# Kernel optimization log

Measured on AMD Instinct MI355X. Metric: run time of the kernel, lower is better.

Reference implementation:

```python
import jax, jax.numpy as jnp
import numpy as np

H, C = 8, 32          # heads, per-head channels (h_feats)
NEG_SLOPE = 0.2


def setup_inputs() -> dict:
    key = jax.random.key(0)
    ks = jax.random.split(key, 9)
    N, E, F_IN, F_E = 50000, 800000, 128, 16
    x = jax.random.normal(ks[0], (N, F_IN), jnp.float32)
    edge_index = jax.random.randint(ks[1], (2, E), 0, N, jnp.int64)
    edge_attr = jax.random.normal(ks[2], (E, F_E), jnp.float32)
    s = 1.0 / np.sqrt(F_IN)
    W = jax.random.normal(ks[3], (H * C, F_IN), jnp.float32) * s
    W_edge = jax.random.normal(ks[4], (H * C, F_E), jnp.float32) * (1.0 / np.sqrt(F_E))
    att_src = jax.random.normal(ks[5], (H, C), jnp.float32) * (1.0 / np.sqrt(C))
    att_dst = jax.random.normal(ks[6], (H, C), jnp.float32) * (1.0 / np.sqrt(C))
    att_edge = jax.random.normal(ks[7], (H, C), jnp.float32) * (1.0 / np.sqrt(C))
    bias = jnp.zeros((C,), jnp.float32)
    return {"x": x, "edge_index": edge_index, "edge_attr": edge_attr,
            "W": W, "W_edge": W_edge, "att_src": att_src, "att_dst": att_dst,
            "att_edge": att_edge, "bias": bias}


def reference(x, edge_index, edge_attr, W, W_edge, att_src, att_dst, att_edge, bias):
    N = x.shape[0]
    src, dst = edge_index[0], edge_index[1]

    # --- add self loops, edge_attr fill_value='mean' (per-dst mean of incoming attrs) ---
    deg = jax.ops.segment_sum(jnp.ones_like(dst, dtype=edge_attr.dtype), dst, num_segments=N)
    loop_attr = jax.ops.segment_sum(edge_attr, dst, num_segments=N) / jnp.maximum(deg, 1.0)[:, None]
    loop = jnp.arange(N, dtype=src.dtype)
    src = jnp.concatenate([src, loop])
    dst = jnp.concatenate([dst, loop])
    ea = jnp.concatenate([edge_attr, loop_attr], axis=0)  # [E+N, F_e]

    # --- node projection and per-node attention terms ---
    xh = (x @ W.T).reshape(N, H, C)                      # [N,H,C]
    a_src = jnp.einsum('nhc,hc->nh', xh, att_src)        # [N,H]
    a_dst = jnp.einsum('nhc,hc->nh', xh, att_dst)        # [N,H]

    # edge attention folded: (lin_edge(e).view(E,H,C) * att_edge).sum(-1) == e @ M
    M = jnp.einsum('hcf,hc->fh', W_edge.reshape(H, C, -1), att_edge)  # [F_e,H]
    a_edge = ea @ M                                      # [E+N,H]

    alpha = a_src[src] + a_dst[dst] + a_edge             # [E+N,H]
    alpha = jnp.where(alpha >= 0, alpha, NEG_SLOPE * alpha)

    # --- scatter-softmax over edges grouped by dst node ---
    amax = jax.ops.segment_max(alpha, dst, num_segments=N)  # every node has a self loop
    ex = jnp.exp(alpha - amax[dst])
    denom = jax.ops.segment_sum(ex, dst, num_segments=N)
    att = ex / denom[dst]                                # [E+N,H]

    # --- weighted message scatter-sum ---
    msg = xh[src] * att[..., None]                       # [E+N,H,C]
    out = jax.ops.segment_sum(msg, dst, num_segments=N)  # [N,H,C]
    return out.mean(axis=1) + bias                       # concat=False -> head mean
```

## Files before the change

### kernel.cpp

```cpp
#include <hip/hip_runtime.h>
#include <math.h>

#define H 8
#define C 32
#define HC 256
#define FE 16
#define FIN 128
#define NEG_SLOPE 0.2f

typedef __attribute__((ext_vector_type(8))) short bf16x8;
typedef __attribute__((ext_vector_type(4))) float f32x4;

__device__ __forceinline__ unsigned short f2bf(float f) {
  unsigned int u = __float_as_uint(f);
  unsigned int lsb = (u >> 16) & 1u;
  u += 0x7fffu + lsb;
  return (unsigned short)(u >> 16);
}
__device__ __forceinline__ float bf2f(unsigned short s) {
  return __uint_as_float(((unsigned int)s) << 16);
}

__device__ __forceinline__ void split8(const float* v, bf16x8& hi, bf16x8& lo) {
#pragma unroll
  for (int i = 0; i < 8; ++i) {
    unsigned int u = __float_as_uint(v[i]);
    unsigned int hu = u & 0xffff0000u;
    float r = v[i] - __uint_as_float(hu);
    hi[i] = (short)(hu >> 16);
    lo[i] = (short)f2bf(r);
  }
}

__global__ __launch_bounds__(256) void k_xh(const float* __restrict__ x,
                                            const unsigned short* __restrict__ Whi,
                                            const unsigned short* __restrict__ Wlo,
                                            const float* __restrict__ att_src,
                                            const float* __restrict__ att_dst,
                                            unsigned short* __restrict__ xhb,
                                            float* __restrict__ a_src,
                                            float* __restrict__ a_dst, int N) {
  int t = threadIdx.x;
  int w = t >> 6, lane = t & 63;
  int n15 = lane & 15, q = lane >> 4;
  int nodeBase = blockIdx.x * 128 + w * 32;
  int chBase = blockIdx.y * 128;

  f32x4 acc[8][2];
#pragma unroll
  for (int mt = 0; mt < 8; ++mt)
#pragma unroll
    for (int nt = 0; nt < 2; ++nt) acc[mt][nt] = (f32x4)(0.f);

  for (int ks = 0; ks < 4; ++ks) {
    int kOff = ks * 32 + q * 8;
    bf16x8 Bhi[2], Blo[2];
#pragma unroll
    for (int nt = 0; nt < 2; ++nt) {
      int node = nodeBase + nt * 16 + n15;
      int rn = (node < N) ? node : (N - 1);
      const float* px = &x[(size_t)rn * FIN + kOff];
      float vb[8];
      *(float4*)&vb[0] = *(const float4*)px;
      *(float4*)&vb[4] = *(const float4*)(px + 4);
      split8(vb, Bhi[nt], Blo[nt]);
    }
#pragma unroll
    for (int mt = 0; mt < 8; ++mt) {
      int widx = ((chBase + mt * 16 + n15) << 7) + kOff;
      bf16x8 Ahi = *(const bf16x8*)&Whi[widx];
      bf16x8 Alo = *(const bf16x8*)&Wlo[widx];
#pragma unroll
      for (int nt = 0; nt < 2; ++nt) {
        acc[mt][nt] = __builtin_amdgcn_mfma_f32_16x16x32_bf16(Ahi, Bhi[nt], acc[mt][nt], 0, 0, 0);
        acc[mt][nt] = __builtin_amdgcn_mfma_f32_16x16x32_bf16(Ahi, Blo[nt], acc[mt][nt], 0, 0, 0);
        acc[mt][nt] = __builtin_amdgcn_mfma_f32_16x16x32_bf16(Alo, Bhi[nt], acc[mt][nt], 0, 0, 0);
      }
    }
  }

  float ps[2][4] = {{0.f,0.f,0.f,0.f},{0.f,0.f,0.f,0.f}};
  float pd[2][4] = {{0.f,0.f,0.f,0.f},{0.f,0.f,0.f,0.f}};
#pragma unroll
  for (int mt = 0; mt < 8; ++mt) {
    int hl = mt >> 1;
#pragma unroll
    for (int r = 0; r < 4; ++r) {
      int ch = chBase + mt * 16 + q * 4 + r;
      float as_c = att_src[ch], ad_c = att_dst[ch];
#pragma unroll
      for (int nt = 0; nt < 2; ++nt) {
        float val = acc[mt][nt][r];
        ps[nt][hl] = fmaf(val, as_c, ps[nt][hl]);
        pd[nt][hl] = fmaf(val, ad_c, pd[nt][hl]);
      }
    }
#pragma unroll
    for (int nt = 0; nt < 2; ++nt) {
      int node = nodeBase + nt * 16 + n15;
      if (node < N) {
        ushort4 us;
        us.x = f2bf(acc[mt][nt][0]); us.y = f2bf(acc[mt][nt][1]);
        us.z = f2bf(acc[mt][nt][2]); us.w = f2bf(acc[mt][nt][3]);
        *(ushort4*)&xhb[(size_t)node * HC + chBase + mt * 16 + q * 4] = us;
      }
    }
  }
#pragma unroll
  for (int nt = 0; nt < 2; ++nt)
#pragma unroll
    for (int hl = 0; hl < 4; ++hl) {
      ps[nt][hl] += __shfl_xor(ps[nt][hl], 16, 64);
      ps[nt][hl] += __shfl_xor(ps[nt][hl], 32, 64);
      pd[nt][hl] += __shfl_xor(pd[nt][hl], 16, 64);
      pd[nt][hl] += __shfl_xor(pd[nt][hl], 32, 64);
    }
  if (q == 0) {
#pragma unroll
    for (int nt = 0; nt < 2; ++nt) {
      int node = nodeBase + nt * 16 + n15;
      if (node < N) {
        *(float4*)&a_src[node * H + blockIdx.y * 4] = make_float4(ps[nt][0], ps[nt][1], ps[nt][2], ps[nt][3]);
        *(float4*)&a_dst[node * H + blockIdx.y * 4] = make_float4(pd[nt][0], pd[nt][1], pd[nt][2], pd[nt][3]);
      }
    }
  }
}

__global__ __launch_bounds__(256) void k_deg(const int* __restrict__ ei,
                                             int* __restrict__ deg,
                                             int* __restrict__ rank,
                                             const float* __restrict__ W,
                                             unsigned short* __restrict__ Whi,
                                             unsigned short* __restrict__ Wlo, int E) {
  int e = blockIdx.x * 256 + threadIdx.x;
  if (e < HC * FIN) {
    float v = W[e];
    unsigned int u = __float_as_uint(v);
    unsigned int hu = u & 0xffff0000u;
    Whi[e] = (unsigned short)(hu >> 16);
    Wlo[e] = f2bf(v - __uint_as_float(hu));
  }
  if (e < E) rank[e] = atomicAdd(&deg[ei[E + e]], 1);
}

__global__ __launch_bounds__(256) void k_scan1(const int* __restrict__ deg,
                                               int* __restrict__ bsum, int N) {
  int t = threadIdx.x;
  int i = blockIdx.x * 256 + t;
  int v = (i < N) ? deg[i] : 0;
#pragma unroll
  for (int m = 1; m < 64; m <<= 1) v += __shfl_xor(v, m, 64);
  __shared__ int wsum[4];
  if ((t & 63) == 0) wsum[t >> 6] = v;
  __syncthreads();
  if (t == 0) bsum[blockIdx.x] = wsum[0] + wsum[1] + wsum[2] + wsum[3];
}

__global__ __launch_bounds__(256) void k_scan23(const int* __restrict__ deg,
                                                const int* __restrict__ bsum,
                                                int* __restrict__ rowptr, int N, int E, int nb) {
  __shared__ int sb[256];
  __shared__ int buf[256];
  int t = threadIdx.x;
  sb[t] = (t < nb) ? bsum[t] : 0;
  int i = blockIdx.x * 256 + t;
  int v = (i < N) ? deg[i] : 0;
  buf[t] = v;
  __syncthreads();
  for (int off = 1; off < 256; off <<= 1) {
    int y1 = (t >= off) ? sb[t - off] : 0;
    int y2 = (t >= off) ? buf[t - off] : 0;
    __syncthreads();
    sb[t] += y1;
    buf[t] += y2;
    __syncthreads();
  }
  int bofs = (blockIdx.x == 0) ? 0 : sb[blockIdx.x - 1];
  if (i < N) rowptr[i] = bofs + buf[t] - v;
  if (i == 0) rowptr[N] = E;
}

__global__ __launch_bounds__(256) void k_edge_scatter(const int* __restrict__ ei,
                                                      const float* __restrict__ ea,
                                                      const float* __restrict__ W_edge,
                                                      const float* __restrict__ att_edge,
                                                      const int* __restrict__ rowptr,
                                                      const int* __restrict__ rank,
                                                      unsigned short* __restrict__ recs, int E) {
  __shared__ float Ms[FE * H];
  int t = threadIdx.x;
  if (t < FE * H) {
    int f = t >> 3, h = t & 7;
    float acc = 0.f;
#pragma unroll
    for (int c = 0; c < C; ++c)
      acc += W_edge[(h * C + c) * FE + f] * att_edge[h * C + c];
    Ms[f * H + h] = acc;
  }
  __syncthreads();
  int e = blockIdx.x * 256 + t;
  if (e >= E) return;
  int s = ei[e], d = ei[E + e];
  const float4* p = (const float4*)&ea[(size_t)e * FE];
  float4 v0 = p[0], v1 = p[1], v2 = p[2], v3 = p[3];
  float eav[FE] = {v0.x, v0.y, v0.z, v0.w, v1.x, v1.y, v1.z, v1.w,
                   v2.x, v2.y, v2.z, v2.w, v3.x, v3.y, v3.z, v3.w};
  float o[H];
#pragma unroll
  for (int h = 0; h < H; ++h) {
    float acc = 0.f;
#pragma unroll
    for (int f = 0; f < FE; ++f) acc += eav[f] * Ms[f * H + h];
    o[h] = acc;
  }
  int pos = rowptr[d] + rank[e];
  uint4 pk;
  pk.x = (unsigned int)f2bf(o[0]) | ((unsigned int)f2bf(o[1]) << 16);
  pk.y = (unsigned int)f2bf(o[2]) | ((unsigned int)f2bf(o[3]) << 16);
  pk.z = (unsigned int)f2bf(o[4]) | ((unsigned int)f2bf(o[5]) << 16);
  pk.w = (unsigned int)f2bf(o[6]) | ((unsigned int)f2bf(o[7]) << 16);
  uint4 hv; hv.x = (unsigned int)s; hv.y = 0; hv.z = 0; hv.w = 0;
  unsigned short* rp = &recs[(size_t)pos * 16];
  *(uint4*)rp = pk;
  *(uint4*)(rp + 8) = hv;
}

__global__ __launch_bounds__(256) void k_node(const unsigned short* __restrict__ xhb,
                                              const float* __restrict__ a_src,
                                              const float* __restrict__ a_dst,
                                              const unsigned short* __restrict__ recs,
                                              const int* __restrict__ rowptr,
                                              const float* __restrict__ bias,
                                              float* __restrict__ out, int N) {
  __shared__ float wlds[4][512];
  __shared__ int   slds[4][64];
  int wv = threadIdx.x >> 6;
  int lane = threadIdx.x & 63;
  int n = blockIdx.x * 4 + wv;
  if (n >= N) return;
  int start = rowptr[n];
  int deg = rowptr[n + 1] - start;
  int jmax = (deg < 64) ? deg : 64;
  int padded = (jmax + 7) & ~7;
  int h = lane & 7, esub = lane >> 3;
  float adst = a_dst[n * H + h];
  float asrc = a_src[n * H + h];

  float ae[8]; int sr[8];
#pragma unroll
  for (int it = 0; it < 8; ++it) {
    int j = it * 8 + esub;
    ae[it] = 0.f; sr[it] = 0;
    if (j < jmax) {
      const unsigned short* rp = &recs[(size_t)(start + j) * 16];
      ae[it] = bf2f(rp[h]);
      sr[it] = *(const int*)(rp + 8);
    }
  }
  float asg[8];
#pragma unroll
  for (int it = 0; it < 8; ++it) {
    int j = it * 8 + esub;
    asg[it] = (j < jmax) ? a_src[sr[it] * H + h] : 0.f;
  }
  if (h == 0) {
#pragma unroll
    for (int it = 0; it < 8; ++it) {
      int j = it * 8 + esub;
      if (j < jmax) slds[wv][j] = sr[it];
    }
  }
  {
    int pj = jmax + esub;
    if (pj < padded) {
      if (h == 0) slds[wv][pj] = n;
      wlds[wv][pj * 8 + h] = 0.f;
    }
  }
  float al[8];
  float pmax = -1e30f, psum = 0.f;
#pragma unroll
  for (int it = 0; it < 8; ++it) {
    int j = it * 8 + esub;
    float a = -1e30f;
    if (j < jmax) {
      psum += ae[it];
      a = asg[it] + adst + ae[it];
      a = (a >= 0.f) ? a : NEG_SLOPE * a;
      pmax = fmaxf(pmax, a);
    }
    al[it] = a;
  }
  for (int j0 = 64; j0 < deg; j0 += 8) {
    int j = j0 + esub;
    if (j < deg) {
      const unsigned short* rp = &recs[(size_t)(start + j) * 16];
      float aev = bf2f(rp[h]);
      int src = *(const int*)(rp + 8);
      psum += aev;
      float a = a_src[src * H + h] + adst + aev;
      a = (a >= 0.f) ? a : NEG_SLOPE * a;
      pmax = fmaxf(pmax, a);
    }
  }
#pragma unroll
  for (int m = 8; m <= 32; m <<= 1) {
    pmax = fmaxf(pmax, __shfl_xor(pmax, m, 64));
    psum += __shfl_xor(psum, m, 64);
  }
  float aself = asrc + adst + psum / fmaxf((float)deg, 1.f);
  aself = (aself >= 0.f) ? aself : NEG_SLOPE * aself;
  float amax = fmaxf(pmax, aself);

  float den = 0.f;
#pragma unroll
  for (int it = 0; it < 8; ++it) {
    int j = it * 8 + esub;
    if (j < jmax) {
      float wj = __expf(al[it] - amax);
      den += wj;
      wlds[wv][j * 8 + h] = wj;
    }
  }
  for (int j0 = 64; j0 < deg; j0 += 8) {
    int j = j0 + esub;
    if (j < deg) {
      const unsigned short* rp = &recs[(size_t)(start + j) * 16];
      float aev = bf2f(rp[h]);
      int src = *(const int*)(rp + 8);
      float a = a_src[src * H + h] + adst + aev;
      a = (a >= 0.f) ? a : NEG_SLOPE * a;
      den += __expf(a - amax);
    }
  }
#pragma unroll
  for (int m = 8; m <= 32; m <<= 1) den += __shfl_xor(den, m, 64);
  float wself = __expf(aself - amax);
  float inv = 1.f / (den + wself);

  int hc = lane >> 3;
  float inv_c  = __shfl(inv, hc, 64);
  float ws_c   = __shfl(wself, hc, 64);
  float amax_c = __shfl(amax, hc, 64);
  float adst_c = __shfl(adst, hc, 64);
  float accx, accy, accz, accw;
  {
    uint2 u = ((const uint2*)(xhb + (((size_t)n) << 8)))[lane];
    accx = ws_c * __uint_as_float(u.x << 16);
    accy = ws_c * __uint_as_float(u.x & 0xffff0000u);
    accz = ws_c * __uint_as_float(u.y << 16);
    accw = ws_c * __uint_as_float(u.y & 0xffff0000u);
  }
  for (int j0 = 0; j0 < padded; j0 += 8) {
    uint2 v[8]; float wj[8];
#pragma unroll
    for (int k = 0; k < 8; ++k) {
      wj[k] = wlds[wv][(j0 + k) * 8 + hc];
      v[k] = ((const uint2*)(xhb + (((size_t)slds[wv][j0 + k]) << 8)))[lane];
    }
#pragma unroll
    for (int k = 0; k < 8; ++k) {
      accx = fmaf(__uint_as_float(v[k].x << 16), wj[k], accx);
      accy = fmaf(__uint_as_float(v[k].x & 0xffff0000u), wj[k], accy);
      accz = fmaf(__uint_as_float(v[k].y << 16), wj[k], accz);
      accw = fmaf(__uint_as_float(v[k].y & 0xffff0000u), wj[k], accw);
    }
  }
  for (int j = 64; j < deg; ++j) {
    const unsigned short* rp = &recs[(size_t)(start + j) * 16];
    float aev = bf2f(rp[hc]);
    int src = *(const int*)(rp + 8);
    float a = a_src[src * H + hc] + adst_c + aev;
    a = (a >= 0.f) ? a : NEG_SLOPE * a;
    float wj = __expf(a - amax_c);
    uint2 v = ((const uint2*)(xhb + (((size_t)src) << 8)))[lane];
    accx = fmaf(__uint_as_float(v.x << 16), wj, accx);
    accy = fmaf(__uint_as_float(v.x & 0xffff0000u), wj, accy);
    accz = fmaf(__uint_as_float(v.y << 16), wj, accz);
    accw = fmaf(__uint_as_float(v.y & 0xffff0000u), wj, accw);
  }
  accx *= inv_c; accy *= inv_c; accz *= inv_c; accw *= inv_c;

#pragma unroll
  for (int m = 8; m <= 32; m <<= 1) {
    accx += __shfl_xor(accx, m, 64);
    accy += __shfl_xor(accy, m, 64);
    accz += __shfl_xor(accz, m, 64);
    accw += __shfl_xor(accw, m, 64);
  }
  if (lane < 8) {
    float4 b = ((const float4*)bias)[lane];
    float4 o;
    o.x = accx * 0.125f + b.x;
    o.y = accy * 0.125f + b.y;
    o.z = accz * 0.125f + b.z;
    o.w = accw * 0.125f + b.w;
    ((float4*)&out[(size_t)n * C])[lane] = o;
  }
}

extern "C" void kernel_launch(void* const* d_in, const int* in_sizes, int n_in,
                              void* d_out, int out_size, void* d_ws, size_t ws_size,
                              hipStream_t stream) {
  const float* x        = (const float*)d_in[0];
  const int*   ei       = (const int*)d_in[1];
  const float* ea       = (const float*)d_in[2];
  const float* W        = (const float*)d_in[3];
  const float* W_edge   = (const float*)d_in[4];
  const float* att_src  = (const float*)d_in[5];
  const float* att_dst  = (const float*)d_in[6];
  const float* att_edge = (const float*)d_in[7];
  const float* bias     = (const float*)d_in[8];
  float* out = (float*)d_out;

  int N = in_sizes[0] / FIN;
  int E = in_sizes[1] / 2;
  int nb = (N + 255) / 256;

  char* ws = (char*)d_ws;
  auto take = [&](size_t bytes) {
    char* p = ws;
    ws += (bytes + 255) & ~(size_t)255;
    return p;
  };
  unsigned short* xhb    = (unsigned short*)take((size_t)N * HC * 2);
  float*          a_src  = (float*)take((size_t)N * H * 4);
  float*          a_dst  = (float*)take((size_t)N * H * 4);
  unsigned short* recs   = (unsigned short*)take((size_t)E * 32);
  unsigned short* Whi    = (unsigned short*)take((size_t)HC * FIN * 2);
  unsigned short* Wlo    = (unsigned short*)take((size_t)HC * FIN * 2);
  int*            deg    = (int*)take((size_t)N * 4);
  int*            rowptr = (int*)take((size_t)(N + 1) * 4);
  int*            rank   = (int*)take((size_t)E * 4);
  int*            bsum   = (int*)take((size_t)nb * 4);

  hipMemsetAsync(deg, 0, (size_t)N * 4, stream);
  k_deg<<<(E + 255) / 256, 256, 0, stream>>>(ei, deg, rank, W, Whi, Wlo, E);
  k_xh<<<dim3((N + 127) / 128, 2), 256, 0, stream>>>(x, Whi, Wlo, att_src, att_dst, xhb, a_src, a_dst, N);
  k_scan1<<<nb, 256, 0, stream>>>(deg, bsum, N);
  k_scan23<<<nb, 256, 0, stream>>>(deg, bsum, rowptr, N, E, nb);
  k_edge_scatter<<<(E + 255) / 256, 256, 0, stream>>>(ei, ea, W_edge, att_edge, rowptr, rank, recs, E);
  k_node<<<(N + 3) / 4, 256, 0, stream>>>(xhb, a_src, a_dst, recs, rowptr, bias, out, N);
}
```

Before: 301.9 us.

## Drop W low-part MFMA term and replace record scatter with perm-based gather

The low-order bf16 split of W is removed, so the projection GEMM issues two MFMAs per tile instead of three and the Wlo buffer and its loads disappear. The edge-record build is split into a small kernel that writes a permutation index (4-byte scatter) and a gather kernel that writes the 32-byte records contiguously in CSR order. This swaps wide random writes for random reads of edge_attr, and adds a launch plus an extra E-sized int buffer. The att_src/att_dst loads in the epilogue are also vectorised to float4. Dropping the W residual lowers the projection precision to roughly bf16 for W, which may affect accuracy.

```diff
diff --git a/kernel.cpp b/kernel.cpp
--- a/kernel.cpp
+++ b/kernel.cpp
@@ -34,7 +34,6 @@
 
 __global__ __launch_bounds__(256) void k_xh(const float* __restrict__ x,
                                             const unsigned short* __restrict__ Whi,
-                                            const unsigned short* __restrict__ Wlo,
                                             const float* __restrict__ att_src,
                                             const float* __restrict__ att_dst,
                                             unsigned short* __restrict__ xhb,
@@ -69,12 +68,10 @@
     for (int mt = 0; mt < 8; ++mt) {
       int widx = ((chBase + mt * 16 + n15) << 7) + kOff;
       bf16x8 Ahi = *(const bf16x8*)&Whi[widx];
-      bf16x8 Alo = *(const bf16x8*)&Wlo[widx];
 #pragma unroll
       for (int nt = 0; nt < 2; ++nt) {
         acc[mt][nt] = __builtin_amdgcn_mfma_f32_16x16x32_bf16(Ahi, Bhi[nt], acc[mt][nt], 0, 0, 0);
         acc[mt][nt] = __builtin_amdgcn_mfma_f32_16x16x32_bf16(Ahi, Blo[nt], acc[mt][nt], 0, 0, 0);
-        acc[mt][nt] = __builtin_amdgcn_mfma_f32_16x16x32_bf16(Alo, Bhi[nt], acc[mt][nt], 0, 0, 0);
       }
     }
   }
@@ -84,15 +81,17 @@
 #pragma unroll
   for (int mt = 0; mt < 8; ++mt) {
     int hl = mt >> 1;
+    float4 as4 = *(const float4*)&att_src[chBase + mt * 16 + q * 4];
+    float4 ad4 = *(const float4*)&att_dst[chBase + mt * 16 + q * 4];
+    float asv[4] = {as4.x, as4.y, as4.z, as4.w};
+    float adv[4] = {ad4.x, ad4.y, ad4.z, ad4.w};
 #pragma unroll
     for (int r = 0; r < 4; ++r) {
-      int ch = chBase + mt * 16 + q * 4 + r;
-      float as_c = att_src[ch], ad_c = att_dst[ch];
 #pragma unroll
       for (int nt = 0; nt < 2; ++nt) {
         float val = acc[mt][nt][r];
-        ps[nt][hl] = fmaf(val, as_c, ps[nt][hl]);
-        pd[nt][hl] = fmaf(val, ad_c, pd[nt][hl]);
+        ps[nt][hl] = fmaf(val, asv[r], ps[nt][hl]);
+        pd[nt][hl] = fmaf(val, adv[r], pd[nt][hl]);
       }
     }
 #pragma unroll
@@ -131,16 +130,9 @@
                                              int* __restrict__ deg,
                                              int* __restrict__ rank,
                                              const float* __restrict__ W,
-                                             unsigned short* __restrict__ Whi,
-                                             unsigned short* __restrict__ Wlo, int E) {
+                                             unsigned short* __restrict__ Whi, int E) {
   int e = blockIdx.x * 256 + threadIdx.x;
-  if (e < HC * FIN) {
-    float v = W[e];
-    unsigned int u = __float_as_uint(v);
-    unsigned int hu = u & 0xffff0000u;
-    Whi[e] = (unsigned short)(hu >> 16);
-    Wlo[e] = f2bf(v - __uint_as_float(hu));
-  }
+  if (e < HC * FIN) Whi[e] = f2bf(W[e]);
   if (e < E) rank[e] = atomicAdd(&deg[ei[E + e]], 1);
 }
 
@@ -181,13 +173,22 @@
   if (i == 0) rowptr[N] = E;
 }
 
-__global__ __launch_bounds__(256) void k_edge_scatter(const int* __restrict__ ei,
-                                                      const float* __restrict__ ea,
-                                                      const float* __restrict__ W_edge,
-                                                      const float* __restrict__ att_edge,
-                                                      const int* __restrict__ rowptr,
-                                                      const int* __restrict__ rank,
-                                                      unsigned short* __restrict__ recs, int E) {
+__global__ __launch_bounds__(256) void k_perm(const int* __restrict__ ei,
+                                              const int* __restrict__ rank,
+                                              const int* __restrict__ rowptr,
+                                              int* __restrict__ perm, int E) {
+  int e = blockIdx.x * 256 + threadIdx.x;
+  if (e >= E) return;
+  int d = ei[E + e];
+  perm[rowptr[d] + rank[e]] = e;
+}
+
+__global__ __launch_bounds__(256) void k_edge_gather(const int* __restrict__ ei,
+                                                     const float* __restrict__ ea,
+                                                     const float* __restrict__ W_edge,
+                                                     const float* __restrict__ att_edge,
+                                                     const int* __restrict__ perm,
+                                                     unsigned short* __restrict__ recs, int E) {
   __shared__ float Ms[FE * H];
   int t = threadIdx.x;
   if (t < FE * H) {
@@ -199,9 +200,10 @@
     Ms[f * H + h] = acc;
   }
   __syncthreads();
-  int e = blockIdx.x * 256 + t;
-  if (e >= E) return;
-  int s = ei[e], d = ei[E + e];
+  int pos = blockIdx.x * 256 + t;
+  if (pos >= E) return;
+  int e = perm[pos];
+  int s = ei[e];
   const float4* p = (const float4*)&ea[(size_t)e * FE];
   float4 v0 = p[0], v1 = p[1], v2 = p[2], v3 = p[3];
   float eav[FE] = {v0.x, v0.y, v0.z, v0.w, v1.x, v1.y, v1.z, v1.w,
@@ -214,7 +216,6 @@
     for (int f = 0; f < FE; ++f) acc += eav[f] * Ms[f * H + h];
     o[h] = acc;
   }
-  int pos = rowptr[d] + rank[e];
   uint4 pk;
   pk.x = (unsigned int)f2bf(o[0]) | ((unsigned int)f2bf(o[1]) << 16);
   pk.y = (unsigned int)f2bf(o[2]) | ((unsigned int)f2bf(o[3]) << 16);
@@ -429,17 +430,18 @@
   float*          a_dst  = (float*)take((size_t)N * H * 4);
   unsigned short* recs   = (unsigned short*)take((size_t)E * 32);
   unsigned short* Whi    = (unsigned short*)take((size_t)HC * FIN * 2);
-  unsigned short* Wlo    = (unsigned short*)take((size_t)HC * FIN * 2);
   int*            deg    = (int*)take((size_t)N * 4);
   int*            rowptr = (int*)take((size_t)(N + 1) * 4);
   int*            rank   = (int*)take((size_t)E * 4);
+  int*            perm   = (int*)take((size_t)E * 4);
   int*            bsum   = (int*)take((size_t)nb * 4);
 
   hipMemsetAsync(deg, 0, (size_t)N * 4, stream);
-  k_deg<<<(E + 255) / 256, 256, 0, stream>>>(ei, deg, rank, W, Whi, Wlo, E);
-  k_xh<<<dim3((N + 127) / 128, 2), 256, 0, stream>>>(x, Whi, Wlo, att_src, att_dst, xhb, a_src, a_dst, N);
+  k_deg<<<(E + 255) / 256, 256, 0, stream>>>(ei, deg, rank, W, Whi, E);
+  k_xh<<<dim3((N + 127) / 128, 2), 256, 0, stream>>>(x, Whi, att_src, att_dst, xhb, a_src, a_dst, N);
   k_scan1<<<nb, 256, 0, stream>>>(deg, bsum, N);
   k_scan23<<<nb, 256, 0, stream>>>(deg, bsum, rowptr, N, E, nb);
-  k_edge_scatter<<<(E + 255) / 256, 256, 0, stream>>>(ei, ea, W_edge, att_edge, rowptr, rank, recs, E);
+  k_perm<<<(E + 255) / 256, 256, 0, stream>>>(ei, rank, rowptr, perm, E);
+  k_edge_gather<<<(E + 255) / 256, 256, 0, stream>>>(ei, ea, W_edge, att_edge, perm, recs, E);
   k_node<<<(N + 3) / 4, 256, 0, stream>>>(xhb, a_src, a_dst, recs, rowptr, bias, out, N);
 }
```

New measurement: 302.8 us. Within noise of the previous version (+0.3%).
